# Performance work log

Measured on AMD Instinct MI355X. Metric: run time of the kernel, lower is better.

Reference implementation:

```python
import jax, jax.numpy as jnp
import numpy as np

N, E = 100000, 1600000          # nodes, edges
DIN, DH, DOUT = 128, 128, 64    # input_dim, hidden_dim, output_dim


def setup_inputs() -> dict:
    key = jax.random.key(0)
    k0, k1, k2, k3 = jax.random.split(key, 4)
    x = jax.random.normal(k0, (N, DIN), dtype=jnp.float32)
    edge_index = jax.random.randint(k1, (2, E), 0, N)
    # GCNConv params (glorot-ish weights, zero bias)
    W1 = jax.random.normal(k2, (DIN, DH), dtype=jnp.float32) / np.sqrt(DIN).astype(np.float32)
    b1 = jnp.zeros((DH,), jnp.float32)
    W2 = jax.random.normal(k3, (DH, DOUT), dtype=jnp.float32) / np.sqrt(DH).astype(np.float32)
    b2 = jnp.zeros((DOUT,), jnp.float32)
    return {"x": x, "edge_index": edge_index, "W1": W1, "b1": b1, "W2": W2, "b2": b2}


def _gcn_conv(h_in, W, b, src, dst, norm_e, self_norm, n):
    # PyG GCNConv: transform, then normalized sum-aggregation with self-loops.
    h = h_in @ W                                   # [N, dout]
    msg = h[src] * norm_e[:, None]                 # [E, dout] gather + edge scale
    agg = jax.ops.segment_sum(msg, dst, num_segments=n)
    agg = agg + h * self_norm[:, None]             # self-loop contribution (norm = 1/deg)
    return agg + b


def reference(x, edge_index, W1, b1, W2, b2):
    src, dst = edge_index[0], edge_index[1]
    n = x.shape[0]
    # degree including self-loop, computed on dst (PyG convention)
    deg = jax.ops.segment_sum(jnp.ones((src.shape[0],), x.dtype), dst, num_segments=n) + 1.0
    dinv = jax.lax.rsqrt(deg)
    norm_e = dinv[src] * dinv[dst]                 # per-edge D^-1/2 A D^-1/2
    self_norm = dinv * dinv
    h = _gcn_conv(x, W1, b1, src, dst, norm_e, self_norm, n)
    h = jax.nn.relu(h)                             # dropout is identity in eval mode
    out = _gcn_conv(h, W2, b2, src, dst, norm_e, self_norm, n)
    return out
```

## Files before the change

kernel.cpp:

```cpp
#include <hip/hip_runtime.h>

#define NN 100000
#define NE 1600000
#define NBUCK 1563
#define NBH 256
#define CHUNK 6250
#define NBXB 12500
#define NBG 1563


typedef short bf16x8 __attribute__((ext_vector_type(8)));
typedef float f32x4  __attribute__((ext_vector_type(4)));
typedef float f32x2  __attribute__((ext_vector_type(2)));

__device__ __forceinline__ float b2f(unsigned short u) {
    return __uint_as_float(((unsigned int)u) << 16);
}
__device__ __forceinline__ unsigned short f2b(float f) {
    unsigned int x = __float_as_uint(f);
    x += 0x7FFFu + ((x >> 16) & 1u);
    return (unsigned short)(x >> 16);
}

__global__ __launch_bounds__(256) void k_pre(const float* __restrict__ x,
                                             unsigned short* __restrict__ xb,
                                             const int* __restrict__ dst,
                                             int* __restrict__ ghist) {
    int b = blockIdx.x;
    if (b < NBXB) {
        int id = b * 256 + threadIdx.x;
        float4 v = ((const float4*)x)[id];
        ushort4 o;
        o.x = f2b(v.x); o.y = f2b(v.y); o.z = f2b(v.z); o.w = f2b(v.w);
        ((ushort4*)xb)[id] = o;
        return;
    }
    __shared__ int h[NBUCK];
    int tid = threadIdx.x;
    int i = b - NBXB;
    for (int k = tid; k < NBUCK; k += 256) h[k] = 0;
    __syncthreads();
    int e0 = i * CHUNK;
    for (int e = e0 + tid; e < e0 + CHUNK; e += 256) {
        unsigned d = (unsigned)dst[e];
        if (d < NN) atomicAdd(&h[d >> 6], 1);
    }
    __syncthreads();
    for (int k = tid; k < NBUCK; k += 256) ghist[i * NBUCK + k] = h[k];
}

__global__ __launch_bounds__(256) void k_scanB(const int* __restrict__ ghist,
                                               int* __restrict__ boffT,
                                               int* __restrict__ tot) {
    int k = blockIdx.x * 256 + threadIdx.x;
    if (k >= NBUCK) return;
    int sum = 0;
#pragma unroll 8
    for (int i = 0; i < NBH; ++i) {
        int c = ghist[i * NBUCK + k];
        boffT[i * NBUCK + k] = sum;
        sum += c;
    }
    tot[k] = sum;
}

__global__ __launch_bounds__(256) void k_scanT(const int* __restrict__ tot,
                                               int* __restrict__ bbase) {
    __shared__ int s[256];
    int tid = threadIdx.x;
    int k0 = tid * 7;
    int v[7]; int S = 0;
#pragma unroll
    for (int q = 0; q < 7; ++q) {
        int k = k0 + q;
        v[q] = (k < NBUCK) ? tot[k] : 0;
        S += v[q];
    }
    s[tid] = S;
    __syncthreads();
    for (int off = 1; off < 256; off <<= 1) {
        int t = (tid >= off) ? s[tid - off] : 0;
        __syncthreads();
        s[tid] += t;
        __syncthreads();
    }
    int run = s[tid] - S;
#pragma unroll
    for (int q = 0; q < 7; ++q) {
        int k = k0 + q;
        if (k < NBUCK) { bbase[k] = run; run += v[q]; }
    }
}

__global__ __launch_bounds__(256) void k_place(const int* __restrict__ src,
                                               const int* __restrict__ dst,
                                               const int* __restrict__ bbase,
                                               const int* __restrict__ boffT,
                                               int* __restrict__ ebuf) {
    __shared__ int cur[NBUCK];
    int tid = threadIdx.x, i = blockIdx.x;
    for (int k = tid; k < NBUCK; k += 256)
        cur[k] = bbase[k] + boffT[i * NBUCK + k];
    __syncthreads();
    int e0 = i * CHUNK;
    for (int e = e0 + tid; e < e0 + CHUNK; e += 256) {
        unsigned d = (unsigned)dst[e];
        if (d >= NN) continue;
        unsigned s = (unsigned)src[e];
        if (s >= NN) s = 0;
        int pos = atomicAdd(&cur[d >> 6], 1);
        ebuf[pos] = (int)(s | ((d & 63u) << 17));
    }
}

__global__ __launch_bounds__(256) void k_binC(const int* __restrict__ bbase,
                                              const int* __restrict__ tot,
                                              const int* __restrict__ ebuf,
                                              int* __restrict__ row_start,
                                              float* __restrict__ dinv,
                                              int* __restrict__ csr) {
    __shared__ int cnt[64], excl[64], cur[64];
    int b = blockIdx.x, tid = threadIdx.x;
    int n0 = b * 64;
    int base = bbase[b], end = base + tot[b];
    if (tid < 64) cnt[tid] = 0;
    __syncthreads();
    for (int i = base + tid; i < end; i += 256)
        atomicAdd(&cnt[((unsigned)ebuf[i]) >> 17], 1);
    __syncthreads();
    if (tid == 0) {
        int run = 0;
        for (int t = 0; t < 64; ++t) { excl[t] = run; run += cnt[t]; }
    }
    __syncthreads();
    if (tid < 64) {
        int node = n0 + tid;
        if (node < NN) {
            row_start[node] = base + excl[tid];
            dinv[node] = rsqrtf((float)cnt[tid] + 1.0f);
        }
        cur[tid] = base + excl[tid];
    }
    if (b == NBUCK - 1 && tid == 0) row_start[NN] = end;
    __syncthreads();
    for (int i = base + tid; i < end; i += 256) {
        unsigned rec = (unsigned)ebuf[i];
        int pos = atomicAdd(&cur[rec >> 17], 1);
        csr[pos] = (int)(rec & 0x1FFFFu);
    }
}

__global__ __launch_bounds__(256) void k_agg1(const unsigned short* __restrict__ xb,
                                              const float* __restrict__ dinv,
                                              const int* __restrict__ row_start,
                                              const int* __restrict__ csr,
                                              char* __restrict__ P) {
    int node = blockIdx.x * 4 + (threadIdx.x >> 6);
    int lane = threadIdx.x & 63;
    float dv = dinv[node]; float sn = dv * dv;
    unsigned int sv = ((const unsigned int*)(xb + (size_t)node * 128))[lane];
    float ax = b2f((unsigned short)(sv & 0xFFFF)) * sn;
    float ay = b2f((unsigned short)(sv >> 16)) * sn;
    int base = row_start[node], end = row_start[node + 1];
    for (int i0 = base; i0 < end; i0 += 64) {
        int idx = i0 + lane;
        int s = (idx < end) ? csr[idx] : 0;
        float wv = (idx < end) ? dinv[s] * dv : 0.f;
        int m = min(64, end - i0);
        int j = 0;
        for (; j + 3 < m; j += 4) {
            int   s0 = __shfl(s, j),  s1 = __shfl(s, j + 1);
            int   s2 = __shfl(s, j + 2), s3 = __shfl(s, j + 3);
            float w0 = __shfl(wv, j), w1 = __shfl(wv, j + 1);
            float w2 = __shfl(wv, j + 2), w3 = __shfl(wv, j + 3);
            unsigned int v0 = ((const unsigned int*)(xb + (size_t)s0 * 128))[lane];
            unsigned int v1 = ((const unsigned int*)(xb + (size_t)s1 * 128))[lane];
            unsigned int v2 = ((const unsigned int*)(xb + (size_t)s2 * 128))[lane];
            unsigned int v3 = ((const unsigned int*)(xb + (size_t)s3 * 128))[lane];
            ax = fmaf(b2f((unsigned short)(v0 & 0xFFFF)), w0, ax);
            ay = fmaf(b2f((unsigned short)(v0 >> 16)),    w0, ay);
            ax = fmaf(b2f((unsigned short)(v1 & 0xFFFF)), w1, ax);
            ay = fmaf(b2f((unsigned short)(v1 >> 16)),    w1, ay);
            ax = fmaf(b2f((unsigned short)(v2 & 0xFFFF)), w2, ax);
            ay = fmaf(b2f((unsigned short)(v2 >> 16)),    w2, ay);
            ax = fmaf(b2f((unsigned short)(v3 & 0xFFFF)), w3, ax);
            ay = fmaf(b2f((unsigned short)(v3 >> 16)),    w3, ay);
        }
        for (; j < m; ++j) {
            int s0 = __shfl(s, j);
            float w0 = __shfl(wv, j);
            unsigned int v0 = ((const unsigned int*)(xb + (size_t)s0 * 128))[lane];
            ax = fmaf(b2f((unsigned short)(v0 & 0xFFFF)), w0, ax);
            ay = fmaf(b2f((unsigned short)(v0 >> 16)),    w0, ay);
        }
    }
    unsigned int o = (unsigned int)f2b(ax) | ((unsigned int)f2b(ay) << 16);
    ((unsigned int*)(P + (size_t)node * 256))[lane] = o;
}

__global__ __launch_bounds__(256) void k_gemm12(const float* __restrict__ W1,
                                                const float* __restrict__ b1,
                                                const float* __restrict__ W2,
                                                char* __restrict__ P) {
    __shared__ short Wl1[16384];
    __shared__ short Wl2[8192];
    __shared__ __align__(16) short Cl[4][16][128];
    const int tid = threadIdx.x;
    const int w = tid >> 6, lane = tid & 63;
    const int r0 = blockIdx.x * 64;

    for (int i = tid; i < 16384; i += 256) {
        int j = i & 7, l = (i >> 3) & 63, ks = (i >> 9) & 3, ct = i >> 11;
        int k = ks * 32 + ((l >> 4) << 3) + j;
        int c = ct * 16 + (l & 15);
        Wl1[i] = (short)f2b(W1[k * 128 + c]);
    }
    for (int i = tid; i < 8192; i += 256) {
        int j = i & 7, l = (i >> 3) & 63, ks = (i >> 9) & 3, ct = i >> 11;
        int k = ks * 32 + ((l >> 4) << 3) + j;
        int c = ct * 16 + (l & 15);
        Wl2[i] = (short)f2b(W2[k * 64 + c]);
    }
    __syncthreads();

    const int m = r0 + w * 16 + (lane & 15);
    const int quad = lane >> 4;
    const bool mok = (m < NN);
    bf16x8 a[4];
#pragma unroll
    for (int ks = 0; ks < 4; ++ks) {
        if (mok) a[ks] = *(const bf16x8*)(P + (size_t)m * 256 + (ks * 32 + quad * 8) * 2);
        else     a[ks] = bf16x8{0,0,0,0,0,0,0,0};
    }
#pragma unroll
    for (int ct = 0; ct < 8; ++ct) {
        f32x4 c = {0.f, 0.f, 0.f, 0.f};
#pragma unroll
        for (int ks = 0; ks < 4; ++ks) {
            bf16x8 b = *(const bf16x8*)&Wl1[((ct * 4 + ks) * 64 + lane) * 8];
            c = __builtin_amdgcn_mfma_f32_16x16x32_bf16(a[ks], b, c, 0, 0, 0);
        }
        int col = ct * 16 + (lane & 15);
        float bias = b1[col];
#pragma unroll
        for (int r = 0; r < 4; ++r)
            Cl[w][quad * 4 + r][col] = (short)f2b(fmaxf(c[r] + bias, 0.f));
    }
    __syncthreads();
    bf16x8 a2[4];
#pragma unroll
    for (int ks = 0; ks < 4; ++ks)
        a2[ks] = *(const bf16x8*)&Cl[w][lane & 15][ks * 32 + quad * 8];
    __syncthreads();
    short* Ct = &Cl[0][0][0];
#pragma unroll
    for (int ct = 0; ct < 4; ++ct) {
        f32x4 c = {0.f, 0.f, 0.f, 0.f};
#pragma unroll
        for (int ks = 0; ks < 4; ++ks) {
            bf16x8 b = *(const bf16x8*)&Wl2[((ct * 4 + ks) * 64 + lane) * 8];
            c = __builtin_amdgcn_mfma_f32_16x16x32_bf16(a2[ks], b, c, 0, 0, 0);
        }
        int col = ct * 16 + (lane & 15);
#pragma unroll
        for (int r = 0; r < 4; ++r)
            Ct[(w * 16 + quad * 4 + r) * 64 + col] = (short)f2b(c[r]);
    }
    __syncthreads();
    for (int it = 0; it < 8; ++it) {
        int row = it * 2 + (lane >> 5), u = lane & 31;
        int node = r0 + w * 16 + row;
        if (node < NN)
            *(unsigned int*)(P + (size_t)node * 256 + u * 4) =
                ((const unsigned int*)&Ct[(w * 16 + row) * 64])[u];
    }
}

__global__ __launch_bounds__(256) void k_agg2(const float* __restrict__ dinv,
                                              const int* __restrict__ row_start,
                                              const int* __restrict__ csr,
                                              const char* __restrict__ P,
                                              const float* __restrict__ b2,
                                              float* __restrict__ outp) {
    int node = blockIdx.x * 4 + (threadIdx.x >> 6);
    int lane = threadIdx.x & 63;
    int sub  = lane >> 3;
    int dimb = lane & 7;
    const uint4* P4 = (const uint4*)P;
    float dv = dinv[node];
    float sn8 = dv * dv * 0.125f;
    uint4 sv = P4[(size_t)node * 16 + dimb];
    f32x2 a0, a1, a2, a3;
    a0.x = __uint_as_float(sv.x << 16) * sn8;  a0.y = __uint_as_float(sv.x & 0xFFFF0000u) * sn8;
    a1.x = __uint_as_float(sv.y << 16) * sn8;  a1.y = __uint_as_float(sv.y & 0xFFFF0000u) * sn8;
    a2.x = __uint_as_float(sv.z << 16) * sn8;  a2.y = __uint_as_float(sv.z & 0xFFFF0000u) * sn8;
    a3.x = __uint_as_float(sv.w << 16) * sn8;  a3.y = __uint_as_float(sv.w & 0xFFFF0000u) * sn8;
    int base = row_start[node], end = row_start[node + 1];
    if (end > base) {
        for (int c0 = base; c0 < end; c0 += 64) {
            int idx = c0 + lane;
            int cl = min(idx, end - 1);
            int s = csr[cl];
            float wv = (idx < end) ? dinv[s] * dv : 0.f;
            int ng = min(64, end - c0);
            for (int g = 0; g * 8 < ng; ++g) {
                int   sq = __shfl(s,  g * 8 + sub);
                float wq = __shfl(wv, g * 8 + sub);
                uint4 v = P4[(size_t)sq * 16 + dimb];
                f32x2 wv2; wv2.x = wq; wv2.y = wq;
                f32x2 xv;
                xv.x = __uint_as_float(v.x << 16); xv.y = __uint_as_float(v.x & 0xFFFF0000u);
                a0 = __builtin_elementwise_fma(xv, wv2, a0);
                xv.x = __uint_as_float(v.y << 16); xv.y = __uint_as_float(v.y & 0xFFFF0000u);
                a1 = __builtin_elementwise_fma(xv, wv2, a1);
                xv.x = __uint_as_float(v.z << 16); xv.y = __uint_as_float(v.z & 0xFFFF0000u);
                a2 = __builtin_elementwise_fma(xv, wv2, a2);
                xv.x = __uint_as_float(v.w << 16); xv.y = __uint_as_float(v.w & 0xFFFF0000u);
                a3 = __builtin_elementwise_fma(xv, wv2, a3);
            }
        }
    }
#pragma unroll
    for (int mgap = 8; mgap < 64; mgap <<= 1) {
        a0.x += __shfl_xor(a0.x, mgap); a0.y += __shfl_xor(a0.y, mgap);
        a1.x += __shfl_xor(a1.x, mgap); a1.y += __shfl_xor(a1.y, mgap);
        a2.x += __shfl_xor(a2.x, mgap); a2.y += __shfl_xor(a2.y, mgap);
        a3.x += __shfl_xor(a3.x, mgap); a3.y += __shfl_xor(a3.y, mgap);
    }
    if (lane < 8) {
        float4 ba = ((const float4*)b2)[lane * 2];
        float4 bb = ((const float4*)b2)[lane * 2 + 1];
        float4 o0, o1;
        o0.x = a0.x + ba.x; o0.y = a0.y + ba.y; o0.z = a1.x + ba.z; o0.w = a1.y + ba.w;
        o1.x = a2.x + bb.x; o1.y = a2.y + bb.y; o1.z = a3.x + bb.z; o1.w = a3.y + bb.w;
        ((float4*)outp)[(size_t)node * 16 + lane * 2]     = o0;
        ((float4*)outp)[(size_t)node * 16 + lane * 2 + 1] = o1;
    }
}

extern "C" void kernel_launch(void* const* d_in, const int* in_sizes, int n_in,
                              void* d_out, int out_size, void* d_ws, size_t ws_size,
                              hipStream_t stream) {
    const float* x  = (const float*)d_in[0];
    const int*   ei = (const int*)d_in[1];
    const float* W1 = (const float*)d_in[2];
    const float* b1 = (const float*)d_in[3];
    const float* W2 = (const float*)d_in[4];
    const float* b2 = (const float*)d_in[5];
    float* out = (float*)d_out;
    const int* src = ei;
    const int* dst = ei + NE;

    char* ws = (char*)d_ws;
    unsigned short* xb        = (unsigned short*)(ws + 0);
    char*           P         = ws + 25600000;
    int*            ghist     = (int*)(ws + 25600000);
    int*            boffT     = (int*)(ws + 27200512);
    int*            tot       = (int*)(ws + 28801024);
    int*            bbase     = (int*)(ws + 28807276);
    int*            row_start = (int*)(ws + 51200000);
    float*          dinv      = (float*)(ws + 51600004);
    int*            csr       = (int*)(ws + 52000004);
    int*            ebuf      = (int*)(ws + 58400004);

    k_pre  <<<NBXB + NBH, 256, 0, stream>>>(x, xb, dst, ghist);
    k_scanB<<<(NBUCK + 255) / 256, 256, 0, stream>>>(ghist, boffT, tot);
    k_scanT<<<1, 256, 0, stream>>>(tot, bbase);
    k_place<<<NBH, 256, 0, stream>>>(src, dst, bbase, boffT, ebuf);
    k_binC <<<NBUCK, 256, 0, stream>>>(bbase, tot, ebuf, row_start, dinv, csr);

    k_agg1  <<<NN / 4, 256, 0, stream>>>(xb, dinv, row_start, csr, P);
    k_gemm12<<<NBG, 256, 0, stream>>>(W1, b1, W2, P);
    k_agg2  <<<NN / 4, 256, 0, stream>>>(dinv, row_start, csr, P, b2, out);
}
```

Measured before the change: 345.2 us.

## Split each wavefront into four edge groups with 16-byte gathers in agg1

The layer-1 aggregation kernel now has each 64-lane wavefront process four neighbor edges at a time. Each 16-lane subgroup gathers one full 256-byte bf16 row with uint4 loads instead of one 4-byte element per lane. Partial sums are combined with an xor-shuffle reduction across subgroups, and only 16 lanes write the output row. This aims to cut per-edge load instructions and serial loop iterations, at the cost of a cross-lane reduction and lanes sitting idle when an edge group is only partly filled.

```diff
diff --git a/kernel.cpp b/kernel.cpp
--- a/kernel.cpp
+++ b/kernel.cpp
@@ -157,45 +157,55 @@
                                               char* __restrict__ P) {
     int node = blockIdx.x * 4 + (threadIdx.x >> 6);
     int lane = threadIdx.x & 63;
-    float dv = dinv[node]; float sn = dv * dv;
-    unsigned int sv = ((const unsigned int*)(xb + (size_t)node * 128))[lane];
-    float ax = b2f((unsigned short)(sv & 0xFFFF)) * sn;
-    float ay = b2f((unsigned short)(sv >> 16)) * sn;
+    int sub  = lane >> 4;
+    int dimb = lane & 15;
+    const uint4* X4 = (const uint4*)xb;
+    float dv = dinv[node];
+    float sn4 = dv * dv * 0.25f;
+    uint4 sv = X4[(size_t)node * 16 + dimb];
+    f32x2 a0, a1, a2, a3;
+    a0.x = __uint_as_float(sv.x << 16) * sn4;  a0.y = __uint_as_float(sv.x & 0xFFFF0000u) * sn4;
+    a1.x = __uint_as_float(sv.y << 16) * sn4;  a1.y = __uint_as_float(sv.y & 0xFFFF0000u) * sn4;
+    a2.x = __uint_as_float(sv.z << 16) * sn4;  a2.y = __uint_as_float(sv.z & 0xFFFF0000u) * sn4;
+    a3.x = __uint_as_float(sv.w << 16) * sn4;  a3.y = __uint_as_float(sv.w & 0xFFFF0000u) * sn4;
     int base = row_start[node], end = row_start[node + 1];
-    for (int i0 = base; i0 < end; i0 += 64) {
-        int idx = i0 + lane;
-        int s = (idx < end) ? csr[idx] : 0;
+    for (int c0 = base; c0 < end; c0 += 64) {
+        int idx = c0 + lane;
+        int cl = min(idx, end - 1);
+        int s = csr[cl];
         float wv = (idx < end) ? dinv[s] * dv : 0.f;
-        int m = min(64, end - i0);
-        int j = 0;
-        for (; j + 3 < m; j += 4) {
-            int   s0 = __shfl(s, j),  s1 = __shfl(s, j + 1);
-            int   s2 = __shfl(s, j + 2), s3 = __shfl(s, j + 3);
-            float w0 = __shfl(wv, j), w1 = __shfl(wv, j + 1);
-            float w2 = __shfl(wv, j + 2), w3 = __shfl(wv, j + 3);
-            unsigned int v0 = ((const unsigned int*)(xb + (size_t)s0 * 128))[lane];
-            unsigned int v1 = ((const unsigned int*)(xb + (size_t)s1 * 128))[lane];
-            unsigned int v2 = ((const unsigned int*)(xb + (size_t)s2 * 128))[lane];
-            unsigned int v3 = ((const unsigned int*)(xb + (size_t)s3 * 128))[lane];
-            ax = fmaf(b2f((unsigned short)(v0 & 0xFFFF)), w0, ax);
-            ay = fmaf(b2f((unsigned short)(v0 >> 16)),    w0, ay);
-            ax = fmaf(b2f((unsigned short)(v1 & 0xFFFF)), w1, ax);
-            ay = fmaf(b2f((unsigned short)(v1 >> 16)),    w1, ay);
-            ax = fmaf(b2f((unsigned short)(v2 & 0xFFFF)), w2, ax);
-            ay = fmaf(b2f((unsigned short)(v2 >> 16)),    w2, ay);
-            ax = fmaf(b2f((unsigned short)(v3 & 0xFFFF)), w3, ax);
-            ay = fmaf(b2f((unsigned short)(v3 >> 16)),    w3, ay);
-        }
-        for (; j < m; ++j) {
-            int s0 = __shfl(s, j);
-            float w0 = __shfl(wv, j);
-            unsigned int v0 = ((const unsigned int*)(xb + (size_t)s0 * 128))[lane];
-            ax = fmaf(b2f((unsigned short)(v0 & 0xFFFF)), w0, ax);
-            ay = fmaf(b2f((unsigned short)(v0 >> 16)),    w0, ay);
-        }
-    }
-    unsigned int o = (unsigned int)f2b(ax) | ((unsigned int)f2b(ay) << 16);
-    ((unsigned int*)(P + (size_t)node * 256))[lane] = o;
+        int ng = min(64, end - c0);
+        for (int g = 0; g * 4 < ng; ++g) {
+            int   sq = __shfl(s,  g * 4 + sub);
+            float wq = __shfl(wv, g * 4 + sub);
+            uint4 v = X4[(size_t)sq * 16 + dimb];
+            f32x2 wv2; wv2.x = wq; wv2.y = wq;
+            f32x2 xv;
+            xv.x = __uint_as_float(v.x << 16); xv.y = __uint_as_float(v.x & 0xFFFF0000u);
+            a0 = __builtin_elementwise_fma(xv, wv2, a0);
+            xv.x = __uint_as_float(v.y << 16); xv.y = __uint_as_float(v.y & 0xFFFF0000u);
+            a1 = __builtin_elementwise_fma(xv, wv2, a1);
+            xv.x = __uint_as_float(v.z << 16); xv.y = __uint_as_float(v.z & 0xFFFF0000u);
+            a2 = __builtin_elementwise_fma(xv, wv2, a2);
+            xv.x = __uint_as_float(v.w << 16); xv.y = __uint_as_float(v.w & 0xFFFF0000u);
+            a3 = __builtin_elementwise_fma(xv, wv2, a3);
+        }
+    }
+#pragma unroll
+    for (int mgap = 16; mgap < 64; mgap <<= 1) {
+        a0.x += __shfl_xor(a0.x, mgap); a0.y += __shfl_xor(a0.y, mgap);
+        a1.x += __shfl_xor(a1.x, mgap); a1.y += __shfl_xor(a1.y, mgap);
+        a2.x += __shfl_xor(a2.x, mgap); a2.y += __shfl_xor(a2.y, mgap);
+        a3.x += __shfl_xor(a3.x, mgap); a3.y += __shfl_xor(a3.y, mgap);
+    }
+    if (lane < 16) {
+        uint4 o;
+        o.x = (unsigned)f2b(a0.x) | ((unsigned)f2b(a0.y) << 16);
+        o.y = (unsigned)f2b(a1.x) | ((unsigned)f2b(a1.y) << 16);
+        o.z = (unsigned)f2b(a2.x) | ((unsigned)f2b(a2.y) << 16);
+        o.w = (unsigned)f2b(a3.x) | ((unsigned)f2b(a3.y) << 16);
+        ((uint4*)(P + (size_t)node * 256))[lane] = o;
+    }
 }
 
 __global__ __launch_bounds__(256) void k_gemm12(const float* __restrict__ W1,
```

Result: no change. 349.4 us (+1.2%).
